# Kernel tuning notes

Measured on AMD Instinct MI355X. Metric: run time of the kernel, lower is better.

## Reference

```python
import jax, jax.numpy as jnp
import numpy as np

EMBED_DIM = 1024
NUM_HEADS = 16
HEAD_DIM = EMBED_DIM // NUM_HEADS


def setup_inputs() -> dict:
    key = jax.random.key(0)
    ks = jax.random.split(key, 9)
    B, S, D = 4, 2048, EMBED_DIM
    s = 1.0 / np.sqrt(D)
    inp = {
        "x": jax.random.normal(ks[0], (B, S, D), dtype=jnp.float32),
        "Wq": jax.random.uniform(ks[1], (D, D), jnp.float32, -s, s),
        "bq": jax.random.uniform(ks[2], (D,), jnp.float32, -s, s),
        "Wk": jax.random.uniform(ks[3], (D, D), jnp.float32, -s, s),
        "bk": jax.random.uniform(ks[4], (D,), jnp.float32, -s, s),
        "Wv": jax.random.uniform(ks[5], (D, D), jnp.float32, -s, s),
        "bv": jax.random.uniform(ks[6], (D,), jnp.float32, -s, s),
        "Wo": jax.random.uniform(ks[7], (D, D), jnp.float32, -s, s),
        "bo": jax.random.uniform(ks[8], (D,), jnp.float32, -s, s),
    }
    return inp


def reference(x, Wq, bq, Wk, bk, Wv, bv, Wo, bo):
    B, S, D = x.shape
    H, Hd = NUM_HEADS, HEAD_DIM
    scale = 1.0 / jnp.sqrt(jnp.asarray(Hd, x.dtype))

    def split_heads(t):  # (B,S,D) -> (B,H,S,Hd)
        return t.reshape(B, S, H, Hd).transpose(0, 2, 1, 3)

    q = split_heads(x @ Wq + bq)
    k = split_heads(x @ Wk + bk)
    v = split_heads(x @ Wv + bv)

    scores = jnp.einsum("bhqd,bhkd->bhqk", q, k) * scale
    attn = jax.nn.softmax(scores, axis=-1)  # dropout is identity in eval mode
    out = jnp.einsum("bhqk,bhkd->bhqd", attn, v)
    out = out.transpose(0, 2, 1, 3).reshape(B, S, D)
    return out @ Wo + bo
```

## Files before the change

### kernel.cpp

```cpp
#include <hip/hip_runtime.h>
#include <cstdint>

typedef unsigned short u16;
typedef uint32_t u32;
typedef float f32x4 __attribute__((ext_vector_type(4)));
typedef short s16x8 __attribute__((ext_vector_type(8)));
typedef u16 u16x4 __attribute__((ext_vector_type(4)));
typedef u32 u32x2 __attribute__((ext_vector_type(2)));
typedef u32 u32x4 __attribute__((ext_vector_type(4)));

__device__ __forceinline__ u16 f2bf(float f) {
  u32 u = __builtin_bit_cast(u32, f);
  u += 0x7FFFu + ((u >> 16) & 1u);
  return (u16)(u >> 16);
}

__device__ __forceinline__ u32 pack2bf_trunc(float lo, float hi) {
  return __builtin_amdgcn_perm(__builtin_bit_cast(u32, hi),
                               __builtin_bit_cast(u32, lo), 0x07060302u);
}

template <typename T>
__device__ __forceinline__ T ldv(const void* p) {
  T v;
  __builtin_memcpy(&v, __builtin_assume_aligned(p, 16), sizeof(T));
  return v;
}

__device__ __forceinline__ void gload_lds16(const void* g, void* l) {
  __builtin_amdgcn_global_load_lds((const __attribute__((address_space(1))) void*)g,
                                   (__attribute__((address_space(3))) void*)l, 16, 0, 0);
}

__global__ __launch_bounds__(256) void cvt_x_k(const float* __restrict__ in,
                                               u16* __restrict__ out) {
  const int i = (blockIdx.x * 256 + threadIdx.x) * 4;
  float4 v = *(const float4*)(in + i);
  u16x4 o;
  o.x = f2bf(v.x); o.y = f2bf(v.y); o.z = f2bf(v.z); o.w = f2bf(v.w);
  *(u16x4*)(out + i) = o;
}

__global__ __launch_bounds__(256) void prep_w_k(const float* __restrict__ Wq,
                                                const float* __restrict__ Wk,
                                                const float* __restrict__ Wv,
                                                const float* __restrict__ Wo,
                                                u16* __restrict__ out) {
  __shared__ u16 t[64][72];
  const float* W = (blockIdx.z == 0) ? Wq : (blockIdx.z == 1) ? Wk
                  : (blockIdx.z == 2) ? Wv : Wo;
  u16* O = out + (size_t)blockIdx.z * 1024 * 1024;
  const int n0 = blockIdx.x * 64, k0 = blockIdx.y * 64;
  const int tid = threadIdx.x;
#pragma unroll
  for (int i = 0; i < 16; ++i) {
    int e = i * 256 + tid;
    int r = e >> 6, c = e & 63;
    t[r][c] = f2bf(W[(size_t)(k0 + r) * 1024 + n0 + c]);
  }
  __syncthreads();
#pragma unroll
  for (int i = 0; i < 16; ++i) {
    int e = i * 256 + tid;
    int rr = e >> 6, cc = e & 63;
    O[(size_t)(n0 + rr) * 1024 + k0 + cc] = t[cc][rr];
  }
}

__global__ __launch_bounds__(256) void gemm_qkv_k(const u16* __restrict__ A,
                                                  const u16* __restrict__ Wt,
                                                  const float* __restrict__ bq,
                                                  const float* __restrict__ bk,
                                                  const float* __restrict__ bv,
                                                  u16* __restrict__ Qh,
                                                  u16* __restrict__ Kh,
                                                  u16* __restrict__ Vt,
                                                  float qscale) {
  constexpr int K = 1024;
  __shared__ __attribute__((aligned(16))) u16 As[128][64];
  __shared__ __attribute__((aligned(16))) u16 Bs[128][64];
  const int tid = threadIdx.x;
  const int l = tid & 63, w = tid >> 6;
  const int lr = l & 15, lg = l >> 4;
  const int m0 = blockIdx.x * 128;
  const int ng = blockIdx.y * 128;
  const int seg = ng >> 10;
  const int n0 = ng & 1023;
  const u16* Bt = Wt + ((size_t)seg << 20);
  const int wr = (w >> 1) * 64, wc = (w & 1) * 64;
  const int rA = tid >> 3;
  const int cA = (tid & 7) * 8;

  f32x4 acc[4][4] = {};

  for (int kt = 0; kt < K; kt += 64) {
#pragma unroll
    for (int i = 0; i < 4; ++i) {
      gload_lds16(A + (size_t)(m0 + i * 32 + rA) * K + kt + cA,
                  &As[0][0] + (size_t)(i * 256 + w * 64) * 8);
      gload_lds16(Bt + (size_t)(n0 + i * 32 + rA) * K + kt + cA,
                  &Bs[0][0] + (size_t)(i * 256 + w * 64) * 8);
    }
    __syncthreads();
#pragma unroll
    for (int kk = 0; kk < 2; ++kk) {
      s16x8 a[4], b[4];
#pragma unroll
      for (int mi = 0; mi < 4; ++mi)
        a[mi] = ldv<s16x8>(&As[wr + mi * 16 + lr][kk * 32 + lg * 8]);
#pragma unroll
      for (int ni = 0; ni < 4; ++ni)
        b[ni] = ldv<s16x8>(&Bs[wc + ni * 16 + lr][kk * 32 + lg * 8]);
#pragma unroll
      for (int mi = 0; mi < 4; ++mi)
#pragma unroll
        for (int ni = 0; ni < 4; ++ni)
          acc[mi][ni] = __builtin_amdgcn_mfma_f32_16x16x32_bf16(a[mi], b[ni], acc[mi][ni], 0, 0, 0);
    }
    __syncthreads();
  }

  const float* bias = (seg == 0) ? bq : (seg == 1) ? bk : bv;
  const float scale = (seg == 0) ? qscale : 1.0f;
  u16* outp = (seg == 0) ? Qh : (seg == 1) ? Kh : Vt;

  u16* Cb = &As[0][0];
  const int bb = m0 >> 11;
  const int sbase = m0 & 2047;

#pragma unroll
  for (int p = 0; p < 2; ++p) {
    __syncthreads();
    if ((wc >> 6) == p) {
#pragma unroll
      for (int ni = 0; ni < 4; ++ni) {
        const int c = ni * 16 + lr;
        const float bvv = bias[n0 + p * 64 + c];
#pragma unroll
        for (int mi = 0; mi < 4; ++mi) {
#pragma unroll
          for (int r = 0; r < 4; ++r) {
            const int row = wr + mi * 16 + lg * 4 + r;
            Cb[row * 64 + ((((c >> 3) ^ (row & 7)) << 3) | (c & 7))] =
                f2bf((acc[mi][ni][r] + bvv) * scale);
          }
        }
      }
    }
    __syncthreads();
    const int h = (n0 + p * 64) >> 6;
    if (seg <= 1) {
      const int row = tid >> 1;
      const int s = sbase + row;
#pragma unroll
      for (int j = 0; j < 4; ++j) {
        const int c = (tid & 1) * 32 + j * 8;
        s16x8 v = ldv<s16x8>(&Cb[row * 64 + (((c >> 3) ^ (row & 7)) << 3)]);
        const int chunk = (seg == 0) ? (c >> 3) : (((c >> 3) ^ (s & 7)) & 7);
        *(s16x8*)(outp + ((size_t)((bb << 4) + h) * 2048 + s) * 64 + (chunk << 3)) = v;
      }
    } else {
      const int hd = tid & 63;
#pragma unroll
      for (int j = 0; j < 4; ++j) {
        const int s0 = ((tid >> 6) * 4 + j) * 8;
        u16 vals[8];
#pragma unroll
        for (int i = 0; i < 8; ++i) {
          const int row = s0 + i;
          vals[i] = Cb[row * 64 + ((((hd >> 3) ^ (row & 7)) << 3) | (hd & 7))];
        }
        const int sl = sbase + s0;
        const int swz = (((sl >> 3) & 7) ^ (hd & 7)) & 7;
        *(s16x8*)(outp + ((size_t)((bb << 4) + h) * 64 + hd) * 2048 +
                  ((sl & ~63) | (swz << 3))) = *(s16x8*)vals;
      }
    }
  }
}

__global__ __launch_bounds__(256) void gemm_o_k(const u16* __restrict__ A,
                                                const u16* __restrict__ Bt,
                                                const float* __restrict__ bias,
                                                float* __restrict__ outp) {
  constexpr int K = 1024;
  __shared__ __attribute__((aligned(16))) u16 As[128][64];
  __shared__ __attribute__((aligned(16))) u16 Bs[128][64];
  const int tid = threadIdx.x;
  const int l = tid & 63, w = tid >> 6;
  const int lr = l & 15, lg = l >> 4;
  const int m0 = blockIdx.x * 128, n0 = blockIdx.y * 128;
  const int wr = (w >> 1) * 64, wc = (w & 1) * 64;
  const int rA = tid >> 3;
  const int cA = (tid & 7) * 8;

  f32x4 acc[4][4] = {};

  for (int kt = 0; kt < K; kt += 64) {
#pragma unroll
    for (int i = 0; i < 4; ++i) {
      gload_lds16(A + (size_t)(m0 + i * 32 + rA) * K + kt + cA,
                  &As[0][0] + (size_t)(i * 256 + w * 64) * 8);
      gload_lds16(Bt + (size_t)(n0 + i * 32 + rA) * K + kt + cA,
                  &Bs[0][0] + (size_t)(i * 256 + w * 64) * 8);
    }
    __syncthreads();
#pragma unroll
    for (int kk = 0; kk < 2; ++kk) {
      s16x8 a[4], b[4];
#pragma unroll
      for (int mi = 0; mi < 4; ++mi)
        a[mi] = ldv<s16x8>(&As[wr + mi * 16 + lr][kk * 32 + lg * 8]);
#pragma unroll
      for (int ni = 0; ni < 4; ++ni)
        b[ni] = ldv<s16x8>(&Bs[wc + ni * 16 + lr][kk * 32 + lg * 8]);
#pragma unroll
      for (int mi = 0; mi < 4; ++mi)
#pragma unroll
        for (int ni = 0; ni < 4; ++ni)
          acc[mi][ni] = __builtin_amdgcn_mfma_f32_16x16x32_bf16(a[mi], b[ni], acc[mi][ni], 0, 0, 0);
    }
    __syncthreads();
  }

#pragma unroll
  for (int ni = 0; ni < 4; ++ni) {
    const int col = n0 + wc + ni * 16 + lr;
    const float bv = bias[col];
#pragma unroll
    for (int mi = 0; mi < 4; ++mi)
#pragma unroll
      for (int r = 0; r < 4; ++r) {
        const int rowm = m0 + wr + mi * 16 + lg * 4 + r;
        outp[(size_t)rowm * 1024 + col] = acc[mi][ni][r] + bv;
      }
  }
}

__global__ __launch_bounds__(256, 4) void attn_k(const u16* __restrict__ Qh,
                                                 const u16* __restrict__ Kg,
                                                 const u16* __restrict__ Vg,
                                                 u16* __restrict__ Oattn) {
  __shared__ __attribute__((aligned(16))) u16 Kbuf[2][4096];
  __shared__ __attribute__((aligned(16))) u16 Vbuf[2][4096];
  __shared__ __attribute__((aligned(16))) u16 P_lds[4][16][64];
  const int tid = threadIdx.x, l = tid & 63, w = tid >> 6;
  const int lr = l & 15, lg = l >> 4;
  const int bh = blockIdx.y;
  const int q0 = blockIdx.x * 128 + w * 32;
  const u16* Q = Qh + (size_t)bh * (2048 * 64);
  const u16* K = Kg + (size_t)bh * (2048 * 64);
  const u16* V = Vg + (size_t)bh * (64 * 2048);

  s16x8 qf[2][2];
#pragma unroll
  for (int f = 0; f < 2; ++f)
#pragma unroll
    for (int kk = 0; kk < 2; ++kk)
      qf[f][kk] = ldv<s16x8>(Q + (size_t)(q0 + f * 16 + lr) * 64 + kk * 32 + lg * 8);

  const u32 one2 = 0x3F803F80u;
  const s16x8 onesv = __builtin_bit_cast(s16x8, (u32x4){one2, one2, one2, one2});

  f32x4 acc[2][4] = {};
  f32x4 lsum[2] = {};

#define STAGE(buf, kv0)                                                                 \
  do {                                                                                  \
    gload_lds16(K + (size_t)(kv0) * 64 + (size_t)tid * 8, &Kbuf[buf][w * 512]);         \
    gload_lds16(K + (size_t)(kv0) * 64 + 2048 + (size_t)tid * 8,                        \
                &Kbuf[buf][2048 + w * 512]);                                            \
    gload_lds16(V + (size_t)(tid >> 3) * 2048 + (kv0) + (tid & 7) * 8,                  \
                &Vbuf[buf][w * 512]);                                                   \
    gload_lds16(V + (size_t)((tid >> 3) + 32) * 2048 + (kv0) + (tid & 7) * 8,           \
                &Vbuf[buf][2048 + w * 512]);                                            \
  } while (0)

  STAGE(0, 0);
  __syncthreads();

  for (int t = 0; t < 32; ++t) {
    const int cur = t & 1;
    if (t < 31) STAGE(cur ^ 1, (t + 1) * 64);

    f32x4 s[2][4] = {};
    __builtin_amdgcn_s_setprio(1);
#pragma unroll
    for (int tt = 0; tt < 4; ++tt) {
      s16x8 k0 = ldv<s16x8>(&Kbuf[cur][(tt * 16 + lr) * 64 + ((lg ^ (lr & 7)) << 3)]);
      s16x8 k1 = ldv<s16x8>(&Kbuf[cur][(tt * 16 + lr) * 64 + (((4 + lg) ^ (lr & 7)) << 3)]);
#pragma unroll
      for (int f = 0; f < 2; ++f) {
        s[f][tt] = __builtin_amdgcn_mfma_f32_16x16x32_bf16(k0, qf[f][0], s[f][tt], 0, 0, 0);
        s[f][tt] = __builtin_amdgcn_mfma_f32_16x16x32_bf16(k1, qf[f][1], s[f][tt], 0, 0, 0);
      }
    }
    __builtin_amdgcn_s_setprio(0);

    s16x8 pf[2][2];
#pragma unroll
    for (int f = 0; f < 2; ++f) {
#pragma unroll
      for (int tt = 0; tt < 4; ++tt)
#pragma unroll
        for (int r = 0; r < 4; ++r)
          s[f][tt][r] = __builtin_amdgcn_exp2f(s[f][tt][r]);
#pragma unroll
      for (int tt = 0; tt < 4; ++tt) {
        u32x2 pw;
        pw.x = pack2bf_trunc(s[f][tt][0], s[f][tt][1]);
        pw.y = pack2bf_trunc(s[f][tt][2], s[f][tt][3]);
        const int off = (((tt * 2 + (lg >> 1)) ^ (lr & 7)) << 3) + ((lg & 1) << 2);
        *(u32x2*)&P_lds[w][lr][off] = pw;
      }
#pragma unroll
      for (int kvc = 0; kvc < 2; ++kvc)
        pf[f][kvc] = ldv<s16x8>(&P_lds[w][lr][((kvc * 4 + lg) ^ (lr & 7)) << 3]);
      lsum[f] = __builtin_amdgcn_mfma_f32_16x16x32_bf16(pf[f][0], onesv, lsum[f], 0, 0, 0);
      lsum[f] = __builtin_amdgcn_mfma_f32_16x16x32_bf16(pf[f][1], onesv, lsum[f], 0, 0, 0);
    }

    __builtin_amdgcn_s_setprio(1);
#pragma unroll
    for (int dt = 0; dt < 4; ++dt) {
      s16x8 v0 = ldv<s16x8>(&Vbuf[cur][(dt * 16 + lr) * 64 + ((lg ^ (lr & 7)) << 3)]);
      s16x8 v1 = ldv<s16x8>(&Vbuf[cur][(dt * 16 + lr) * 64 + (((4 + lg) ^ (lr & 7)) << 3)]);
#pragma unroll
      for (int f = 0; f < 2; ++f) {
        acc[f][dt] = __builtin_amdgcn_mfma_f32_16x16x32_bf16(pf[f][0], v0, acc[f][dt], 0, 0, 0);
        acc[f][dt] = __builtin_amdgcn_mfma_f32_16x16x32_bf16(pf[f][1], v1, acc[f][dt], 0, 0, 0);
      }
    }
    __builtin_amdgcn_s_setprio(0);
    __syncthreads();
  }
#undef STAGE

  const int b = bh >> 4, h = bh & 15;
#pragma unroll
  for (int f = 0; f < 2; ++f) {
    float li[4];
#pragma unroll
    for (int r = 0; r < 4; ++r) li[r] = __builtin_amdgcn_rcpf(lsum[f][r]);
#pragma unroll
    for (int dt = 0; dt < 4; ++dt)
#pragma unroll
      for (int r = 0; r < 4; ++r) {
        const int q = q0 + f * 16 + lg * 4 + r;
        Oattn[(size_t)((b << 11) + q) * 1024 + (h << 6) + dt * 16 + lr] =
            f2bf(acc[f][dt][r] * li[r]);
      }
  }
}

extern "C" void kernel_launch(void* const* d_in, const int* in_sizes, int n_in,
                              void* d_out, int out_size, void* d_ws, size_t ws_size,
                              hipStream_t stream) {
  const float* x  = (const float*)d_in[0];
  const float* Wq = (const float*)d_in[1];
  const float* bq = (const float*)d_in[2];
  const float* Wk = (const float*)d_in[3];
  const float* bk = (const float*)d_in[4];
  const float* Wv = (const float*)d_in[5];
  const float* bv = (const float*)d_in[6];
  const float* Wo = (const float*)d_in[7];
  const float* bo = (const float*)d_in[8];

  char* ws = (char*)d_ws;
  const size_t MB = 1u << 20;
  u16* xb = (u16*)(ws);
  u16* wt = (u16*)(ws + 16 * MB);
  u16* Qh = (u16*)(ws + 24 * MB);
  u16* Kh = (u16*)(ws + 40 * MB);
  u16* Vt = (u16*)(ws + 56 * MB);
  u16* attn = xb;

  const float qscale = 0.125f * 1.44269504088896f;

  cvt_x_k<<<dim3(8192), dim3(256), 0, stream>>>(x, xb);
  prep_w_k<<<dim3(16, 16, 4), dim3(256), 0, stream>>>(Wq, Wk, Wv, Wo, wt);
  gemm_qkv_k<<<dim3(64, 24), dim3(256), 0, stream>>>(xb, wt, bq, bk, bv, Qh, Kh, Vt, qscale);
  attn_k<<<dim3(16, 64), dim3(256), 0, stream>>>(Qh, Kh, Vt, attn);
  gemm_o_k<<<dim3(64, 8), dim3(256), 0, stream>>>(attn, wt + 3 * 1048576, bo, (float*)d_out);
}
```

Measured before the change: 211.8 us.

## Double-buffer GEMM LDS tiles and use partial vmcnt waits in attention

```diff
diff --git a/kernel.cpp b/kernel.cpp
--- a/kernel.cpp
+++ b/kernel.cpp
@@ -77,8 +77,8 @@
                                                   u16* __restrict__ Vt,
                                                   float qscale) {
   constexpr int K = 1024;
-  __shared__ __attribute__((aligned(16))) u16 As[128][64];
-  __shared__ __attribute__((aligned(16))) u16 Bs[128][64];
+  __shared__ __attribute__((aligned(16))) u16 As[2][128][64];
+  __shared__ __attribute__((aligned(16))) u16 Bs[2][128][64];
   const int tid = threadIdx.x;
   const int l = tid & 63, w = tid >> 6;
   const int lr = l & 15, lg = l >> 4;
@@ -93,38 +93,54 @@
 
   f32x4 acc[4][4] = {};
 
-  for (int kt = 0; kt < K; kt += 64) {
-#pragma unroll
-    for (int i = 0; i < 4; ++i) {
-      gload_lds16(A + (size_t)(m0 + i * 32 + rA) * K + kt + cA,
-                  &As[0][0] + (size_t)(i * 256 + w * 64) * 8);
-      gload_lds16(Bt + (size_t)(n0 + i * 32 + rA) * K + kt + cA,
-                  &Bs[0][0] + (size_t)(i * 256 + w * 64) * 8);
-    }
-    __syncthreads();
+#define GSTAGE(buf, kt)                                                         \
+  do {                                                                          \
+    _Pragma("unroll")                                                           \
+    for (int i = 0; i < 4; ++i) {                                               \
+      gload_lds16(A + (size_t)(m0 + i * 32 + rA) * K + (kt) + cA,               \
+                  &As[buf][0][0] + (size_t)(i * 256 + w * 64) * 8);             \
+      gload_lds16(Bt + (size_t)(n0 + i * 32 + rA) * K + (kt) + cA,              \
+                  &Bs[buf][0][0] + (size_t)(i * 256 + w * 64) * 8);             \
+    }                                                                           \
+  } while (0)
+
+  GSTAGE(0, 0);
+  for (int ki = 0; ki < 16; ++ki) {
+    const int cur = ki & 1;
+    if (ki < 15) {
+      GSTAGE(cur ^ 1, (ki + 1) * 64);
+      asm volatile("s_waitcnt vmcnt(8)" ::: "memory");
+    } else {
+      asm volatile("s_waitcnt vmcnt(0)" ::: "memory");
+    }
+    __builtin_amdgcn_sched_barrier(0);
+    __builtin_amdgcn_s_barrier();
+    __builtin_amdgcn_sched_barrier(0);
 #pragma unroll
     for (int kk = 0; kk < 2; ++kk) {
       s16x8 a[4], b[4];
 #pragma unroll
       for (int mi = 0; mi < 4; ++mi)
-        a[mi] = ldv<s16x8>(&As[wr + mi * 16 + lr][kk * 32 + lg * 8]);
+        a[mi] = ldv<s16x8>(&As[cur][wr + mi * 16 + lr][kk * 32 + lg * 8]);
 #pragma unroll
       for (int ni = 0; ni < 4; ++ni)
-        b[ni] = ldv<s16x8>(&Bs[wc + ni * 16 + lr][kk * 32 + lg * 8]);
+        b[ni] = ldv<s16x8>(&Bs[cur][wc + ni * 16 + lr][kk * 32 + lg * 8]);
 #pragma unroll
       for (int mi = 0; mi < 4; ++mi)
 #pragma unroll
         for (int ni = 0; ni < 4; ++ni)
           acc[mi][ni] = __builtin_amdgcn_mfma_f32_16x16x32_bf16(a[mi], b[ni], acc[mi][ni], 0, 0, 0);
     }
-    __syncthreads();
-  }
+    __builtin_amdgcn_sched_barrier(0);
+    __builtin_amdgcn_s_barrier();
+  }
+#undef GSTAGE
 
   const float* bias = (seg == 0) ? bq : (seg == 1) ? bk : bv;
   const float scale = (seg == 0) ? qscale : 1.0f;
   u16* outp = (seg == 0) ? Qh : (seg == 1) ? Kh : Vt;
 
-  u16* Cb = &As[0][0];
+  u16* Cb = &As[0][0][0];
   const int bb = m0 >> 11;
   const int sbase = m0 & 2047;
 
@@ -184,8 +200,8 @@
                                                 const float* __restrict__ bias,
                                                 float* __restrict__ outp) {
   constexpr int K = 1024;
-  __shared__ __attribute__((aligned(16))) u16 As[128][64];
-  __shared__ __attribute__((aligned(16))) u16 Bs[128][64];
+  __shared__ __attribute__((aligned(16))) u16 As[2][128][64];
+  __shared__ __attribute__((aligned(16))) u16 Bs[2][128][64];
   const int tid = threadIdx.x;
   const int l = tid & 63, w = tid >> 6;
   const int lr = l & 15, lg = l >> 4;
@@ -196,32 +212,48 @@
 
   f32x4 acc[4][4] = {};
 
-  for (int kt = 0; kt < K; kt += 64) {
-#pragma unroll
-    for (int i = 0; i < 4; ++i) {
-      gload_lds16(A + (size_t)(m0 + i * 32 + rA) * K + kt + cA,
-                  &As[0][0] + (size_t)(i * 256 + w * 64) * 8);
-      gload_lds16(Bt + (size_t)(n0 + i * 32 + rA) * K + kt + cA,
-                  &Bs[0][0] + (size_t)(i * 256 + w * 64) * 8);
-    }
-    __syncthreads();
+#define GSTAGE(buf, kt)                                                         \
+  do {                                                                          \
+    _Pragma("unroll")                                                           \
+    for (int i = 0; i < 4; ++i) {                                               \
+      gload_lds16(A + (size_t)(m0 + i * 32 + rA) * K + (kt) + cA,               \
+                  &As[buf][0][0] + (size_t)(i * 256 + w * 64) * 8);             \
+      gload_lds16(Bt + (size_t)(n0 + i * 32 + rA) * K + (kt) + cA,              \
+                  &Bs[buf][0][0] + (size_t)(i * 256 + w * 64) * 8);             \
+    }                                                                           \
+  } while (0)
+
+  GSTAGE(0, 0);
+  for (int ki = 0; ki < 16; ++ki) {
+    const int cur = ki & 1;
+    if (ki < 15) {
+      GSTAGE(cur ^ 1, (ki + 1) * 64);
+      asm volatile("s_waitcnt vmcnt(8)" ::: "memory");
+    } else {
+      asm volatile("s_waitcnt vmcnt(0)" ::: "memory");
+    }
+    __builtin_amdgcn_sched_barrier(0);
+    __builtin_amdgcn_s_barrier();
+    __builtin_amdgcn_sched_barrier(0);
 #pragma unroll
     for (int kk = 0; kk < 2; ++kk) {
       s16x8 a[4], b[4];
 #pragma unroll
       for (int mi = 0; mi < 4; ++mi)
-        a[mi] = ldv<s16x8>(&As[wr + mi * 16 + lr][kk * 32 + lg * 8]);
+        a[mi] = ldv<s16x8>(&As[cur][wr + mi * 16 + lr][kk * 32 + lg * 8]);
 #pragma unroll
       for (int ni = 0; ni < 4; ++ni)
-        b[ni] = ldv<s16x8>(&Bs[wc + ni * 16 + lr][kk * 32 + lg * 8]);
+        b[ni] = ldv<s16x8>(&Bs[cur][wc + ni * 16 + lr][kk * 32 + lg * 8]);
 #pragma unroll
       for (int mi = 0; mi < 4; ++mi)
 #pragma unroll
         for (int ni = 0; ni < 4; ++ni)
           acc[mi][ni] = __builtin_amdgcn_mfma_f32_16x16x32_bf16(a[mi], b[ni], acc[mi][ni], 0, 0, 0);
     }
-    __syncthreads();
-  }
+    __builtin_amdgcn_sched_barrier(0);
+    __builtin_amdgcn_s_barrier();
+  }
+#undef GSTAGE
 
 #pragma unroll
   for (int ni = 0; ni < 4; ++ni) {
@@ -277,11 +309,18 @@
   } while (0)
 
   STAGE(0, 0);
-  __syncthreads();
 
   for (int t = 0; t < 32; ++t) {
     const int cur = t & 1;
-    if (t < 31) STAGE(cur ^ 1, (t + 1) * 64);
+    if (t < 31) {
+      STAGE(cur ^ 1, (t + 1) * 64);
+      asm volatile("s_waitcnt vmcnt(4)" ::: "memory");
+    } else {
+      asm volatile("s_waitcnt vmcnt(0)" ::: "memory");
+    }
+    __builtin_amdgcn_sched_barrier(0);
+    __builtin_amdgcn_s_barrier();
+    __builtin_amdgcn_sched_barrier(0);
 
     f32x4 s[2][4] = {};
     __builtin_amdgcn_s_setprio(1);
@@ -332,7 +371,8 @@
       }
     }
     __builtin_amdgcn_s_setprio(0);
-    __syncthreads();
+    __builtin_amdgcn_sched_barrier(0);
+    __builtin_amdgcn_s_barrier();
   }
 #undef STAGE
 
```

Result: no change. 212.9 us (+0.5%).
